# Optimization experiments

Hardware: AMD Instinct MI355X
Metric: run time of the kernel (lower is better)

## Reference

```python
import jax, jax.numpy as jnp
import numpy as np

BATCH, BITS, HID = 65536, 64, 512
EPS = 1e-5

# M[s, i, j] = 1 if j == i - s  (left-shift-by-s permutation, causal)
_SHIFT_M = jnp.asarray(
    (np.arange(BITS)[None, :, None] - np.arange(BITS)[:, None, None]
     == np.arange(BITS)[None, None, :]).astype(np.float32))


def _layernorm(x, g, b):
    m = jnp.mean(x, axis=-1, keepdims=True)
    v = jnp.var(x, axis=-1, keepdims=True)
    return (x - m) * jax.lax.rsqrt(v + EPS) * g + b


def setup_inputs() -> dict:
    key = jax.random.key(0)
    ks = jax.random.split(key, 8)
    inp = {
        'a_bits': jax.random.uniform(ks[0], (BATCH, BITS), dtype=jnp.float32),
        'shift_bits': jax.random.uniform(ks[1], (BATCH, BITS), dtype=jnp.float32),
        # shift_decoder params: Linear(64,512) -> LN -> GELU -> Linear(512,512) -> LN -> GELU -> Linear(512,64)
        'W1': jax.random.normal(ks[2], (BITS, HID), dtype=jnp.float32) * (1.0 / np.sqrt(BITS)),
        'b1': jnp.zeros((HID,), jnp.float32),
        'g1': jnp.ones((HID,), jnp.float32),
        'be1': jnp.zeros((HID,), jnp.float32),
        'W2': jax.random.normal(ks[3], (HID, HID), dtype=jnp.float32) * (1.0 / np.sqrt(HID)),
        'b2': jnp.zeros((HID,), jnp.float32),
        'g2': jnp.ones((HID,), jnp.float32),
        'be2': jnp.zeros((HID,), jnp.float32),
        'W3': jax.random.normal(ks[4], (HID, BITS), dtype=jnp.float32) * (1.0 / np.sqrt(HID)),
        'b3': jnp.zeros((BITS,), jnp.float32),
    }
    return inp


def reference(a_bits, shift_bits, W1, b1, g1, be1, W2, b2, g2, be2, W3, b3):
    temperature = jnp.float32(1.0)
    # shift decoder MLP
    h = jax.nn.gelu(_layernorm(shift_bits @ W1 + b1, g1, be1), approximate=False)
    h = jax.nn.gelu(_layernorm(h @ W2 + b2, g2, be2), approximate=False)
    shift_logits = (h @ W3 + b3)[:, :BITS]
    # training path: soft shift distribution
    shift_probs = jax.nn.softmax(shift_logits / temperature, axis=-1)
    # weighted permutation matrix, then batched matvec (faithful to einsum+bmm)
    M_weighted = jnp.einsum('bs,sij->bij', shift_probs, _SHIFT_M)
    output = jnp.einsum('bij,bj->bi', M_weighted, a_bits)
    return output
```

## Files before the change

### kernel.cpp

```cpp
#include <hip/hip_runtime.h>
#include <hip/hip_bf16.h>
#include <math.h>

#define BATCH 65536
#define NT 512
#define BM 32

using f32x4 = __attribute__((ext_vector_type(4))) float;
using s16x8 = __attribute__((ext_vector_type(8))) short;

#define MFMA16(a, b, c) __builtin_amdgcn_mfma_f32_16x16x32_bf16((a), (b), (c), 0, 0, 0)

__device__ __forceinline__ unsigned short f2bf(float f) {
    unsigned u = __builtin_bit_cast(unsigned, f);
    u = u + 0x7FFFu + ((u >> 16) & 1u);
    return (unsigned short)(u >> 16);
}

__device__ __forceinline__ float fast_erf(float x) {
    float ax = fabsf(x);
    float t = __builtin_amdgcn_rcpf(fmaf(0.3275911f, ax, 1.0f));
    float poly = t * fmaf(t, fmaf(t, fmaf(t, fmaf(t, 1.061405429f, -1.453152027f),
                                          1.421413741f), -0.284496736f), 0.254829592f);
    float r = 1.0f - poly * __expf(-ax * ax);
    return copysignf(r, x);
}
__device__ __forceinline__ float gelu(float y) {
    return 0.5f * y * (1.0f + fast_erf(y * 0.70710678118654752f));
}

__device__ __forceinline__ int hswz(int row, int k) {
    return row * 1024 + ((((k >> 3) ^ (row & 7))) << 4) + ((k & 7) << 1);
}
__device__ __forceinline__ int xaddr(int base, int row, int k) {
    return base + row * 128 + ((((k >> 3) ^ (row & 7))) << 4) + ((k & 7) << 1);
}

__global__ void weights_frag(const float* __restrict__ W1, const float* __restrict__ W2,
                             const float* __restrict__ W3, unsigned short* __restrict__ wt) {
    int b = blockIdx.x;
    int lane = threadIdx.x;
    const float* src; unsigned short* dst; int N, fragidx;
    if (b < 64)       { src = W1; dst = wt;          N = 512; fragidx = b; }
    else if (b < 576) { src = W2; dst = wt + 32768;  N = 512; fragidx = b - 64; }
    else              { src = W3; dst = wt + 294912; N = 64;  fragidx = b - 576; }
    int nt, ks;
    if (b < 64) { nt = fragidx >> 1; ks = fragidx & 1; }
    else        { nt = fragidx >> 4; ks = fragidx & 15; }
    int n  = nt * 16 + (lane & 15);
    int k0 = ks * 32 + (lane >> 4) * 8;
    unsigned short o[8];
#pragma unroll
    for (int e = 0; e < 8; e++) o[e] = f2bf(src[(size_t)(k0 + e) * N + n]);
    *(uint4*)(dst + ((size_t)fragidx * 64 + lane) * 8) = *(uint4*)o;
}

__device__ __forceinline__ void ln_partials(f32x4 (&acc)[2][4], char* smem, int redb,
                                            int ln, int g, int wave) {
#pragma unroll
    for (int fm = 0; fm < 2; fm++)
#pragma unroll
        for (int r = 0; r < 4; r++) {
            float s = 0.f, q = 0.f;
#pragma unroll
            for (int fn = 0; fn < 4; fn++) { float v = acc[fm][fn][r]; s += v; q += v * v; }
#pragma unroll
            for (int m = 1; m < 16; m <<= 1) { s += __shfl_xor(s, m, 64); q += __shfl_xor(q, m, 64); }
            if (ln == 0) {
                int row = fm * 16 + g * 4 + r;
                float* rp = (float*)(smem + redb + (row * 8 + wave) * 8);
                rp[0] = s; rp[1] = q;
            }
        }
}

#define SMEM_K123 39168
__global__ __launch_bounds__(NT, 4) void k123_fused(
    const float* __restrict__ shift_bits, const float* __restrict__ a_bits,
    const float* __restrict__ b1, const float* __restrict__ g1, const float* __restrict__ be1,
    const float* __restrict__ b2, const float* __restrict__ g2, const float* __restrict__ be2,
    const float* __restrict__ b3, const unsigned short* __restrict__ wt,
    float* __restrict__ out) {
    __shared__ char smem[SMEM_K123];
    const int t = threadIdx.x;
    const int wave = t >> 6, lane = t & 63, g = lane >> 4, ln = lane & 15;
    const int row0 = blockIdx.x * BM;
    const int n0w = wave * 64;
    const int XB = 32768, RB = 36864, SB = 38912;

    {
        int r = t >> 4, c = t & 15;
        float4 x = *(const float4*)(shift_bits + (size_t)(row0 + r) * 64 + c * 4);
        unsigned p0 = (unsigned)f2bf(x.x) | ((unsigned)f2bf(x.y) << 16);
        unsigned p1 = (unsigned)f2bf(x.z) | ((unsigned)f2bf(x.w) << 16);
        uint2 v; v.x = p0; v.y = p1;
        *(uint2*)(smem + XB + r * 128 + (((c >> 1) ^ (r & 7)) << 4) + (c & 1) * 8) = v;
    }
    __syncthreads();

    const unsigned short* w1base = wt + ((size_t)wave * 8 * 64 + lane) * 8;
    f32x4 acc[2][4];
#pragma unroll
    for (int fm = 0; fm < 2; fm++)
#pragma unroll
        for (int fn = 0; fn < 4; fn++) acc[fm][fn] = (f32x4){0.f, 0.f, 0.f, 0.f};
#pragma unroll
    for (int ks = 0; ks < 2; ks++) {
        s16x8 af[2], bf[4];
#pragma unroll
        for (int fn = 0; fn < 4; fn++)
            bf[fn] = *(const s16x8*)(w1base + (size_t)(fn * 2 + ks) * 512);
#pragma unroll
        for (int fm = 0; fm < 2; fm++)
            af[fm] = *(const s16x8*)(smem + xaddr(XB, fm * 16 + ln, ks * 32 + g * 8));
#pragma unroll
        for (int fm = 0; fm < 2; fm++)
#pragma unroll
            for (int fn = 0; fn < 4; fn++) acc[fm][fn] = MFMA16(af[fm], bf[fn], acc[fm][fn]);
    }

    {
        float bb[4];
#pragma unroll
        for (int fn = 0; fn < 4; fn++) bb[fn] = b1[n0w + fn * 16 + ln];
#pragma unroll
        for (int fm = 0; fm < 2; fm++)
#pragma unroll
            for (int fn = 0; fn < 4; fn++)
#pragma unroll
                for (int r = 0; r < 4; r++) acc[fm][fn][r] += bb[fn];
    }
    ln_partials(acc, smem, RB, ln, g, wave);
    __syncthreads();
    if (t < 32) {
        float s = 0.f, q = 0.f;
#pragma unroll
        for (int w = 0; w < 8; w++) {
            float* rp = (float*)(smem + RB + (t * 8 + w) * 8);
            s += rp[0]; q += rp[1];
        }
        float mu = s * (1.0f / 512.0f);
        float var = q * (1.0f / 512.0f) - mu * mu;
        float rs = rsqrtf(var + 1e-5f);
        float* sp = (float*)(smem + SB + t * 8);
        sp[0] = mu; sp[1] = rs;
    }
    __syncthreads();
    {
        float gm[4], bt[4];
#pragma unroll
        for (int fn = 0; fn < 4; fn++) { int c = n0w + fn * 16 + ln; gm[fn] = g1[c]; bt[fn] = be1[c]; }
#pragma unroll
        for (int fm = 0; fm < 2; fm++)
#pragma unroll
            for (int r = 0; r < 4; r++) {
                int row = fm * 16 + g * 4 + r;
                float* sp = (float*)(smem + SB + row * 8);
                float mu = sp[0], rs = sp[1];
#pragma unroll
                for (int fn = 0; fn < 4; fn++) {
                    int col = n0w + fn * 16 + ln;
                    float y = (acc[fm][fn][r] - mu) * rs * gm[fn] + bt[fn];
                    *(unsigned short*)(smem + hswz(row, col)) = f2bf(gelu(y));
                }
            }
    }
    __syncthreads();

    const unsigned short* w2base = wt + 32768 + ((size_t)wave * 64 * 64 + lane) * 8;
#pragma unroll
    for (int fm = 0; fm < 2; fm++)
#pragma unroll
        for (int fn = 0; fn < 4; fn++) acc[fm][fn] = (f32x4){0.f, 0.f, 0.f, 0.f};
#pragma unroll
    for (int step = 0; step < 16; step++) {
        s16x8 bf[4], af[2];
#pragma unroll
        for (int fn = 0; fn < 4; fn++)
            bf[fn] = *(const s16x8*)(w2base + (size_t)(fn * 16 + step) * 512);
#pragma unroll
        for (int fm = 0; fm < 2; fm++)
            af[fm] = *(const s16x8*)(smem + hswz(fm * 16 + ln, step * 32 + g * 8));
#pragma unroll
        for (int fm = 0; fm < 2; fm++)
#pragma unroll
            for (int fn = 0; fn < 4; fn++) acc[fm][fn] = MFMA16(af[fm], bf[fn], acc[fm][fn]);
    }

    {
        float bb[4];
#pragma unroll
        for (int fn = 0; fn < 4; fn++) bb[fn] = b2[n0w + fn * 16 + ln];
#pragma unroll
        for (int fm = 0; fm < 2; fm++)
#pragma unroll
            for (int fn = 0; fn < 4; fn++)
#pragma unroll
                for (int r = 0; r < 4; r++) acc[fm][fn][r] += bb[fn];
    }
    ln_partials(acc, smem, RB, ln, g, wave);
    __syncthreads();
    if (t < 32) {
        float s = 0.f, q = 0.f;
#pragma unroll
        for (int w = 0; w < 8; w++) {
            float* rp = (float*)(smem + RB + (t * 8 + w) * 8);
            s += rp[0]; q += rp[1];
        }
        float mu = s * (1.0f / 512.0f);
        float var = q * (1.0f / 512.0f) - mu * mu;
        float rs = rsqrtf(var + 1e-5f);
        float* sp = (float*)(smem + SB + t * 8);
        sp[0] = mu; sp[1] = rs;
    }
    __syncthreads();
    {
        float gm[4], bt[4];
#pragma unroll
        for (int fn = 0; fn < 4; fn++) { int c = n0w + fn * 16 + ln; gm[fn] = g2[c]; bt[fn] = be2[c]; }
#pragma unroll
        for (int fm = 0; fm < 2; fm++)
#pragma unroll
            for (int r = 0; r < 4; r++) {
                int row = fm * 16 + g * 4 + r;
                float* sp = (float*)(smem + SB + row * 8);
                float mu = sp[0], rs = sp[1];
#pragma unroll
                for (int fn = 0; fn < 4; fn++) {
                    int col = n0w + fn * 16 + ln;
                    float y = (acc[fm][fn][r] - mu) * rs * gm[fn] + bt[fn];
                    *(unsigned short*)(smem + hswz(row, col)) = f2bf(gelu(y));
                }
            }
    }
    __syncthreads();

    const int mh = wave >> 2, q = wave & 3;
    float b3v = b3[q * 16 + ln];
    const unsigned short* b3p = wt + 294912 + ((size_t)q * 16 * 64 + lane) * 8;
    f32x4 acc3a = (f32x4){0.f, 0.f, 0.f, 0.f};
    f32x4 acc3b = (f32x4){0.f, 0.f, 0.f, 0.f};
#pragma unroll
    for (int ks = 0; ks < 16; ks += 2) {
        s16x8 bfr0 = *(const s16x8*)(b3p + (size_t)ks * 512);
        s16x8 bfr1 = *(const s16x8*)(b3p + (size_t)(ks + 1) * 512);
        s16x8 af0 = *(const s16x8*)(smem + hswz(mh * 16 + ln, ks * 32 + g * 8));
        s16x8 af1 = *(const s16x8*)(smem + hswz(mh * 16 + ln, (ks + 1) * 32 + g * 8));
        acc3a = MFMA16(af0, bfr0, acc3a);
        acc3b = MFMA16(af1, bfr1, acc3b);
    }
    __syncthreads();

    const int LOGB = 0, ABUF = 8704, LST = 272, AST = 544;
#pragma unroll
    for (int r = 0; r < 4; r++) {
        int row = mh * 16 + g * 4 + r;
        *(float*)(smem + LOGB + row * LST + (q * 16 + ln) * 4) = acc3a[r] + acc3b[r] + b3v;
    }
    {
        int r = t >> 4, c0 = (t & 15) * 4;
        float* ap = (float*)(smem + ABUF + r * AST);
        float4 z4 = {0.f, 0.f, 0.f, 0.f};
        *(float4*)(ap + c0) = z4;
        float4 av = *(const float4*)(a_bits + (size_t)(row0 + r) * 64 + c0);
        *(float4*)(ap + 64 + c0) = av;
    }
    __syncthreads();

    {
        int r = t >> 4, c0 = (t & 15) * 4;
        float* lp = (float*)(smem + LOGB + r * LST + c0 * 4);
        float4 v = *(float4*)lp;
        float mx = fmaxf(fmaxf(v.x, v.y), fmaxf(v.z, v.w));
#pragma unroll
        for (int d = 1; d < 16; d <<= 1) mx = fmaxf(mx, __shfl_xor(mx, d, 64));
        float e0 = __expf(v.x - mx), e1 = __expf(v.y - mx);
        float e2 = __expf(v.z - mx), e3 = __expf(v.w - mx);
        float s = e0 + e1 + e2 + e3;
#pragma unroll
        for (int d = 1; d < 16; d <<= 1) s += __shfl_xor(s, d, 64);
        float inv = 1.0f / s;
        float4 o; o.x = e0 * inv; o.y = e1 * inv; o.z = e2 * inv; o.w = e3 * inv;
        *(float4*)lp = o;
    }
    __syncthreads();

    {
        int r = t >> 4, i0 = (t & 15) * 4;
        const float* prow = (const float*)(smem + LOGB + r * LST);
        const float* apad = (const float*)(smem + ABUF + r * AST);
        float W[8];
        {
            float4 wa = *(const float4*)(apad + i0 + 60);
            float4 wb = *(const float4*)(apad + i0 + 64);
            W[0] = wa.x; W[1] = wa.y; W[2] = wa.z; W[3] = wa.w;
            W[4] = wb.x; W[5] = wb.y; W[6] = wb.z; W[7] = wb.w;
        }
        float o0 = 0.f, o1 = 0.f, o2 = 0.f, o3 = 0.f;
#pragma unroll
        for (int s4 = 0; s4 < 16; s4++) {
            float4 p4 = *(const float4*)(prow + 4 * s4);
            o0 = fmaf(p4.x, W[4], fmaf(p4.y, W[3], fmaf(p4.z, W[2], fmaf(p4.w, W[1], o0))));
            o1 = fmaf(p4.x, W[5], fmaf(p4.y, W[4], fmaf(p4.z, W[3], fmaf(p4.w, W[2], o1))));
            o2 = fmaf(p4.x, W[6], fmaf(p4.y, W[5], fmaf(p4.z, W[4], fmaf(p4.w, W[3], o2))));
            o3 = fmaf(p4.x, W[7], fmaf(p4.y, W[6], fmaf(p4.z, W[5], fmaf(p4.w, W[4], o3))));
            if (s4 < 15) {
                W[4] = W[0]; W[5] = W[1]; W[6] = W[2]; W[7] = W[3];
                float4 nw = *(const float4*)(apad + i0 + 56 - 4 * s4);
                W[0] = nw.x; W[1] = nw.y; W[2] = nw.z; W[3] = nw.w;
            }
        }
        float4 o; o.x = o0; o.y = o1; o.z = o2; o.w = o3;
        *(float4*)(out + (size_t)(row0 + r) * 64 + i0) = o;
    }
}

extern "C" void kernel_launch(void* const* d_in, const int* in_sizes, int n_in,
                              void* d_out, int out_size, void* d_ws, size_t ws_size,
                              hipStream_t stream) {
    const float* a_bits = (const float*)d_in[0];
    const float* shift  = (const float*)d_in[1];
    const float* W1  = (const float*)d_in[2];
    const float* b1  = (const float*)d_in[3];
    const float* g1  = (const float*)d_in[4];
    const float* be1 = (const float*)d_in[5];
    const float* W2  = (const float*)d_in[6];
    const float* b2  = (const float*)d_in[7];
    const float* g2  = (const float*)d_in[8];
    const float* be2 = (const float*)d_in[9];
    const float* W3  = (const float*)d_in[10];
    const float* b3  = (const float*)d_in[11];
    float* out = (float*)d_out;
    unsigned short* wt = (unsigned short*)d_ws;

    weights_frag<<<640, 64, 0, stream>>>(W1, W2, W3, wt);
    k123_fused<<<BATCH / BM, NT, 0, stream>>>(shift, a_bits, b1, g1, be1,
                                              b2, g2, be2, b3, wt, out);
}
```

Before: 138.9 us.

## Halve block row tile to 16 and raise occupancy to 6 blocks per CU

Each block now processes 16 rows instead of 32, cutting per-wave accumulators in half and shrinking shared memory so launch bounds can ask for 6 blocks per CU. The last-layer GEMM runs on 4 waves while the other 4 waves stage a_bits in parallel, and the softmax and shift stages use only half the threads. Each W2/W3 fragment loaded from global or L2 is now reused across half as many rows, roughly doubling weight traffic per output row.

```diff
diff --git a/kernel.cpp b/kernel.cpp
--- a/kernel.cpp
+++ b/kernel.cpp
@@ -4,7 +4,7 @@
 
 #define BATCH 65536
 #define NT 512
-#define BM 32
+#define BM 16
 
 using f32x4 = __attribute__((ext_vector_type(4))) float;
 using s16x8 = __attribute__((ext_vector_type(8))) short;
@@ -31,9 +31,6 @@
 
 __device__ __forceinline__ int hswz(int row, int k) {
     return row * 1024 + ((((k >> 3) ^ (row & 7))) << 4) + ((k & 7) << 1);
-}
-__device__ __forceinline__ int xaddr(int base, int row, int k) {
-    return base + row * 128 + ((((k >> 3) ^ (row & 7))) << 4) + ((k & 7) << 1);
 }
 
 __global__ void weights_frag(const float* __restrict__ W1, const float* __restrict__ W2,
@@ -55,68 +52,49 @@
     *(uint4*)(dst + ((size_t)fragidx * 64 + lane) * 8) = *(uint4*)o;
 }
 
-__device__ __forceinline__ void ln_partials(f32x4 (&acc)[2][4], char* smem, int redb,
-                                            int ln, int g, int wave) {
-#pragma unroll
-    for (int fm = 0; fm < 2; fm++)
-#pragma unroll
-        for (int r = 0; r < 4; r++) {
-            float s = 0.f, q = 0.f;
-#pragma unroll
-            for (int fn = 0; fn < 4; fn++) { float v = acc[fm][fn][r]; s += v; q += v * v; }
-#pragma unroll
-            for (int m = 1; m < 16; m <<= 1) { s += __shfl_xor(s, m, 64); q += __shfl_xor(q, m, 64); }
-            if (ln == 0) {
-                int row = fm * 16 + g * 4 + r;
-                float* rp = (float*)(smem + redb + (row * 8 + wave) * 8);
-                rp[0] = s; rp[1] = q;
-            }
-        }
-}
-
-#define SMEM_K123 39168
-__global__ __launch_bounds__(NT, 4) void k123_fused(
+#define XB 16384
+#define RB 18432
+#define SB 19456
+#define LOGB 19584
+#define APAD 23936
+#define LST 272
+#define AST 544
+#define SMEM_K 32640
+__global__ __launch_bounds__(NT, 6) void k123_fused(
     const float* __restrict__ shift_bits, const float* __restrict__ a_bits,
     const float* __restrict__ b1, const float* __restrict__ g1, const float* __restrict__ be1,
     const float* __restrict__ b2, const float* __restrict__ g2, const float* __restrict__ be2,
     const float* __restrict__ b3, const unsigned short* __restrict__ wt,
     float* __restrict__ out) {
-    __shared__ char smem[SMEM_K123];
+    __shared__ char smem[SMEM_K];
     const int t = threadIdx.x;
     const int wave = t >> 6, lane = t & 63, g = lane >> 4, ln = lane & 15;
     const int row0 = blockIdx.x * BM;
     const int n0w = wave * 64;
-    const int XB = 32768, RB = 36864, SB = 38912;
-
-    {
-        int r = t >> 4, c = t & 15;
-        float4 x = *(const float4*)(shift_bits + (size_t)(row0 + r) * 64 + c * 4);
-        unsigned p0 = (unsigned)f2bf(x.x) | ((unsigned)f2bf(x.y) << 16);
-        unsigned p1 = (unsigned)f2bf(x.z) | ((unsigned)f2bf(x.w) << 16);
-        uint2 v; v.x = p0; v.y = p1;
-        *(uint2*)(smem + XB + r * 128 + (((c >> 1) ^ (r & 7)) << 4) + (c & 1) * 8) = v;
+
+    {
+        int r = t >> 5, c2 = (t & 31) * 2;
+        float2 x = *(const float2*)(shift_bits + (size_t)(row0 + r) * 64 + c2);
+        unsigned p = (unsigned)f2bf(x.x) | ((unsigned)f2bf(x.y) << 16);
+        *(unsigned*)(smem + XB + r * 128 + (((c2 >> 3) ^ (r & 7)) << 4) + ((c2 & 7) << 1)) = p;
     }
     __syncthreads();
 
     const unsigned short* w1base = wt + ((size_t)wave * 8 * 64 + lane) * 8;
-    f32x4 acc[2][4];
-#pragma unroll
-    for (int fm = 0; fm < 2; fm++)
-#pragma unroll
-        for (int fn = 0; fn < 4; fn++) acc[fm][fn] = (f32x4){0.f, 0.f, 0.f, 0.f};
+    f32x4 acc[4];
+#pragma unroll
+    for (int fn = 0; fn < 4; fn++) acc[fn] = (f32x4){0.f, 0.f, 0.f, 0.f};
 #pragma unroll
     for (int ks = 0; ks < 2; ks++) {
-        s16x8 af[2], bf[4];
+        s16x8 bf[4];
 #pragma unroll
         for (int fn = 0; fn < 4; fn++)
             bf[fn] = *(const s16x8*)(w1base + (size_t)(fn * 2 + ks) * 512);
-#pragma unroll
-        for (int fm = 0; fm < 2; fm++)
-            af[fm] = *(const s16x8*)(smem + xaddr(XB, fm * 16 + ln, ks * 32 + g * 8));
-#pragma unroll
-        for (int fm = 0; fm < 2; fm++)
-#pragma unroll
-            for (int fn = 0; fn < 4; fn++) acc[fm][fn] = MFMA16(af[fm], bf[fn], acc[fm][fn]);
+        s16x8 af = *(const s16x8*)(smem + XB + ln * 128 +
+                                   ((((ks * 32 + g * 8) >> 3) ^ (ln & 7)) << 4) +
+                                   (((ks * 32 + g * 8) & 7) << 1));
+#pragma unroll
+        for (int fn = 0; fn < 4; fn++) acc[fn] = MFMA16(af, bf[fn], acc[fn]);
     }
 
     {
@@ -124,15 +102,25 @@
 #pragma unroll
         for (int fn = 0; fn < 4; fn++) bb[fn] = b1[n0w + fn * 16 + ln];
 #pragma unroll
-        for (int fm = 0; fm < 2; fm++)
-#pragma unroll
-            for (int fn = 0; fn < 4; fn++)
-#pragma unroll
-                for (int r = 0; r < 4; r++) acc[fm][fn][r] += bb[fn];
-    }
-    ln_partials(acc, smem, RB, ln, g, wave);
-    __syncthreads();
-    if (t < 32) {
+        for (int fn = 0; fn < 4; fn++)
+#pragma unroll
+            for (int r = 0; r < 4; r++) acc[fn][r] += bb[fn];
+#pragma unroll
+        for (int r = 0; r < 4; r++) {
+            float s = 0.f, q = 0.f;
+#pragma unroll
+            for (int fn = 0; fn < 4; fn++) { float v = acc[fn][r]; s += v; q += v * v; }
+#pragma unroll
+            for (int m = 1; m < 16; m <<= 1) { s += __shfl_xor(s, m, 64); q += __shfl_xor(q, m, 64); }
+            if (ln == 0) {
+                int row = g * 4 + r;
+                float* rp = (float*)(smem + RB + (row * 8 + wave) * 8);
+                rp[0] = s; rp[1] = q;
+            }
+        }
+    }
+    __syncthreads();
+    if (t < 16) {
         float s = 0.f, q = 0.f;
 #pragma unroll
         for (int w = 0; w < 8; w++) {
@@ -151,40 +139,32 @@
 #pragma unroll
         for (int fn = 0; fn < 4; fn++) { int c = n0w + fn * 16 + ln; gm[fn] = g1[c]; bt[fn] = be1[c]; }
 #pragma unroll
-        for (int fm = 0; fm < 2; fm++)
-#pragma unroll
-            for (int r = 0; r < 4; r++) {
-                int row = fm * 16 + g * 4 + r;
-                float* sp = (float*)(smem + SB + row * 8);
-                float mu = sp[0], rs = sp[1];
-#pragma unroll
-                for (int fn = 0; fn < 4; fn++) {
-                    int col = n0w + fn * 16 + ln;
-                    float y = (acc[fm][fn][r] - mu) * rs * gm[fn] + bt[fn];
-                    *(unsigned short*)(smem + hswz(row, col)) = f2bf(gelu(y));
-                }
-            }
+        for (int r = 0; r < 4; r++) {
+            int row = g * 4 + r;
+            float* sp = (float*)(smem + SB + row * 8);
+            float mu = sp[0], rs = sp[1];
+#pragma unroll
+            for (int fn = 0; fn < 4; fn++) {
+                int col = n0w + fn * 16 + ln;
+                float y = (acc[fn][r] - mu) * rs * gm[fn] + bt[fn];
+                *(unsigned short*)(smem + hswz(row, col)) = f2bf(gelu(y));
+            }
+        }
     }
     __syncthreads();
 
     const unsigned short* w2base = wt + 32768 + ((size_t)wave * 64 * 64 + lane) * 8;
 #pragma unroll
-    for (int fm = 0; fm < 2; fm++)
-#pragma unroll
-        for (int fn = 0; fn < 4; fn++) acc[fm][fn] = (f32x4){0.f, 0.f, 0.f, 0.f};
+    for (int fn = 0; fn < 4; fn++) acc[fn] = (f32x4){0.f, 0.f, 0.f, 0.f};
 #pragma unroll
     for (int step = 0; step < 16; step++) {
-        s16x8 bf[4], af[2];
+        s16x8 bf[4];
 #pragma unroll
         for (int fn = 0; fn < 4; fn++)
             bf[fn] = *(const s16x8*)(w2base + (size_t)(fn * 16 + step) * 512);
-#pragma unroll
-        for (int fm = 0; fm < 2; fm++)
-            af[fm] = *(const s16x8*)(smem + hswz(fm * 16 + ln, step * 32 + g * 8));
-#pragma unroll
-        for (int fm = 0; fm < 2; fm++)
-#pragma unroll
-            for (int fn = 0; fn < 4; fn++) acc[fm][fn] = MFMA16(af[fm], bf[fn], acc[fm][fn]);
+        s16x8 af = *(const s16x8*)(smem + hswz(ln, step * 32 + g * 8));
+#pragma unroll
+        for (int fn = 0; fn < 4; fn++) acc[fn] = MFMA16(af, bf[fn], acc[fn]);
     }
 
     {
@@ -192,15 +172,25 @@
 #pragma unroll
         for (int fn = 0; fn < 4; fn++) bb[fn] = b2[n0w + fn * 16 + ln];
 #pragma unroll
-        for (int fm = 0; fm < 2; fm++)
-#pragma unroll
-            for (int fn = 0; fn < 4; fn++)
-#pragma unroll
-                for (int r = 0; r < 4; r++) acc[fm][fn][r] += bb[fn];
-    }
-    ln_partials(acc, smem, RB, ln, g, wave);
-    __syncthreads();
-    if (t < 32) {
+        for (int fn = 0; fn < 4; fn++)
+#pragma unroll
+            for (int r = 0; r < 4; r++) acc[fn][r] += bb[fn];
+#pragma unroll
+        for (int r = 0; r < 4; r++) {
+            float s = 0.f, q = 0.f;
+#pragma unroll
+            for (int fn = 0; fn < 4; fn++) { float v = acc[fn][r]; s += v; q += v * v; }
+#pragma unroll
+            for (int m = 1; m < 16; m <<= 1) { s += __shfl_xor(s, m, 64); q += __shfl_xor(q, m, 64); }
+            if (ln == 0) {
+                int row = g * 4 + r;
+                float* rp = (float*)(smem + RB + (row * 8 + wave) * 8);
+                rp[0] = s; rp[1] = q;
+            }
+        }
+    }
+    __syncthreads();
+    if (t < 16) {
         float s = 0.f, q = 0.f;
 #pragma unroll
         for (int w = 0; w < 8; w++) {
@@ -219,47 +209,44 @@
 #pragma unroll
         for (int fn = 0; fn < 4; fn++) { int c = n0w + fn * 16 + ln; gm[fn] = g2[c]; bt[fn] = be2[c]; }
 #pragma unroll
-        for (int fm = 0; fm < 2; fm++)
-#pragma unroll
-            for (int r = 0; r < 4; r++) {
-                int row = fm * 16 + g * 4 + r;
-                float* sp = (float*)(smem + SB + row * 8);
-                float mu = sp[0], rs = sp[1];
-#pragma unroll
-                for (int fn = 0; fn < 4; fn++) {
-                    int col = n0w + fn * 16 + ln;
-                    float y = (acc[fm][fn][r] - mu) * rs * gm[fn] + bt[fn];
-                    *(unsigned short*)(smem + hswz(row, col)) = f2bf(gelu(y));
-                }
-            }
-    }
-    __syncthreads();
-
-    const int mh = wave >> 2, q = wave & 3;
-    float b3v = b3[q * 16 + ln];
-    const unsigned short* b3p = wt + 294912 + ((size_t)q * 16 * 64 + lane) * 8;
-    f32x4 acc3a = (f32x4){0.f, 0.f, 0.f, 0.f};
-    f32x4 acc3b = (f32x4){0.f, 0.f, 0.f, 0.f};
-#pragma unroll
-    for (int ks = 0; ks < 16; ks += 2) {
-        s16x8 bfr0 = *(const s16x8*)(b3p + (size_t)ks * 512);
-        s16x8 bfr1 = *(const s16x8*)(b3p + (size_t)(ks + 1) * 512);
-        s16x8 af0 = *(const s16x8*)(smem + hswz(mh * 16 + ln, ks * 32 + g * 8));
-        s16x8 af1 = *(const s16x8*)(smem + hswz(mh * 16 + ln, (ks + 1) * 32 + g * 8));
-        acc3a = MFMA16(af0, bfr0, acc3a);
-        acc3b = MFMA16(af1, bfr1, acc3b);
-    }
-    __syncthreads();
-
-    const int LOGB = 0, ABUF = 8704, LST = 272, AST = 544;
-#pragma unroll
-    for (int r = 0; r < 4; r++) {
-        int row = mh * 16 + g * 4 + r;
-        *(float*)(smem + LOGB + row * LST + (q * 16 + ln) * 4) = acc3a[r] + acc3b[r] + b3v;
-    }
-    {
-        int r = t >> 4, c0 = (t & 15) * 4;
-        float* ap = (float*)(smem + ABUF + r * AST);
+        for (int r = 0; r < 4; r++) {
+            int row = g * 4 + r;
+            float* sp = (float*)(smem + SB + row * 8);
+            float mu = sp[0], rs = sp[1];
+#pragma unroll
+            for (int fn = 0; fn < 4; fn++) {
+                int col = n0w + fn * 16 + ln;
+                float y = (acc[fn][r] - mu) * rs * gm[fn] + bt[fn];
+                *(unsigned short*)(smem + hswz(row, col)) = f2bf(gelu(y));
+            }
+        }
+    }
+    __syncthreads();
+
+    if (wave < 4) {
+        const int q = wave;
+        float b3v = b3[q * 16 + ln];
+        const unsigned short* b3p = wt + 294912 + ((size_t)q * 16 * 64 + lane) * 8;
+        f32x4 acc3a = (f32x4){0.f, 0.f, 0.f, 0.f};
+        f32x4 acc3b = (f32x4){0.f, 0.f, 0.f, 0.f};
+#pragma unroll
+        for (int ks = 0; ks < 16; ks += 2) {
+            s16x8 bfr0 = *(const s16x8*)(b3p + (size_t)ks * 512);
+            s16x8 bfr1 = *(const s16x8*)(b3p + (size_t)(ks + 1) * 512);
+            s16x8 af0 = *(const s16x8*)(smem + hswz(ln, ks * 32 + g * 8));
+            s16x8 af1 = *(const s16x8*)(smem + hswz(ln, (ks + 1) * 32 + g * 8));
+            acc3a = MFMA16(af0, bfr0, acc3a);
+            acc3b = MFMA16(af1, bfr1, acc3b);
+        }
+#pragma unroll
+        for (int r = 0; r < 4; r++) {
+            int row = g * 4 + r;
+            *(float*)(smem + LOGB + row * LST + (q * 16 + ln) * 4) = acc3a[r] + acc3b[r] + b3v;
+        }
+    } else {
+        int idx = t - 256;
+        int r = idx >> 4, c0 = (idx & 15) * 4;
+        float* ap = (float*)(smem + APAD + r * AST);
         float4 z4 = {0.f, 0.f, 0.f, 0.f};
         *(float4*)(ap + c0) = z4;
         float4 av = *(const float4*)(a_bits + (size_t)(row0 + r) * 64 + c0);
@@ -267,7 +254,7 @@
     }
     __syncthreads();
 
-    {
+    if (t < 256) {
         int r = t >> 4, c0 = (t & 15) * 4;
         float* lp = (float*)(smem + LOGB + r * LST + c0 * 4);
         float4 v = *(float4*)lp;
@@ -285,10 +272,10 @@
     }
     __syncthreads();
 
-    {
+    if (t < 256) {
         int r = t >> 4, i0 = (t & 15) * 4;
         const float* prow = (const float*)(smem + LOGB + r * LST);
-        const float* apad = (const float*)(smem + ABUF + r * AST);
+        const float* apad = (const float*)(smem + APAD + r * AST);
         float W[8];
         {
             float4 wa = *(const float4*)(apad + i0 + 60);
```

After: 164.1 us. +18.2%, slower.
